# Optimization experiments

Measured on AMD Instinct MI355X. Metric: run time of the kernel, lower is better.

Reference implementation:

```python
import jax, jax.numpy as jnp
import numpy as np

D, H, DH = 64, 4, 32
INNER = H * DH
SCALE = 1.0 / np.sqrt(DH)


def _layernorm(x, w, b, eps=1e-5):
    mu = jnp.mean(x, axis=-1, keepdims=True)
    var = jnp.var(x, axis=-1, keepdims=True)
    return (x - mu) * jax.lax.rsqrt(var + eps) * w + b


def setup_inputs() -> dict:
    key = jax.random.key(0)
    ks = jax.random.split(key, 8)
    B, N = 1, 256
    z = jax.random.normal(ks[0], (B, N, N, D), dtype=jnp.float32)
    mask = jax.random.randint(ks[1], (B, N, N), 0, 2).astype(jnp.bool_)
    ln_w = jnp.ones((D,), jnp.float32)
    ln_b = jnp.zeros((D,), jnp.float32)
    w_qkv = jax.random.normal(ks[2], (3 * INNER, D), jnp.float32) * 0.02
    w_bias = jax.random.normal(ks[3], (H, D), jnp.float32) * 0.02
    w_out = jax.random.normal(ks[4], (D, INNER), jnp.float32) * 0.02
    w_gate = jax.random.normal(ks[5], (INNER, D), jnp.float32) * 0.02
    return {"z": z, "mask": mask, "ln_w": ln_w, "ln_b": ln_b,
            "w_qkv": w_qkv, "w_bias": w_bias, "w_out": w_out, "w_gate": w_gate}


def reference(z, mask, ln_w, ln_b, w_qkv, w_bias, w_out, w_gate):
    # mode == 'starting': attend along the second pair axis per row n.
    B, N = z.shape[0], z.shape[1]
    h = _layernorm(z, ln_w, ln_b)                       # [B,N,N,D]
    qkv = jnp.einsum('bijd,ed->bije', h, w_qkv)         # [B,N,N,3*INNER]
    qkv = qkv.reshape(B, N, N, 3, H, DH)
    q, k, v = qkv[..., 0, :, :], qkv[..., 1, :, :], qkv[..., 2, :, :]  # [B,N,N,H,dh]
    attn = jnp.einsum('bnihd,bnjhd->bnhij', q, k) * SCALE  # [B,N,H,N,N]
    bias = jnp.einsum('bijd,hd->bhij', h, w_bias)          # [B,H,N,N]
    attn = attn + bias[:, None]                            # broadcast over n
    big_neg = jnp.finfo(attn.dtype).min
    attn = jnp.where(mask[:, :, None, None, :], attn, big_neg)  # mask keys j per (b,n)
    attn = jax.nn.softmax(attn, axis=-1)
    out = jnp.einsum('bnhij,bnjhd->bnihd', attn, v)        # [B,N,N,H,dh]
    out = out.reshape(B, N, N, INNER)
    gate = jax.nn.sigmoid(jnp.einsum('bijd,ed->bije', h, w_gate))
    out = jnp.einsum('bije,de->bijd', out * gate, w_out)
    return out
```

## Files before the change

### kernel.cpp

```cpp
#include <hip/hip_runtime.h>
#include <hip/hip_bf16.h>

#define N_ 256
#define D_ 64
#define H_ 4
#define DH_ 32
#define EQKV 384
#define NPOS 65536
#define SCALE_F 0.17677669529663687f
#define BIG_NEG -3.402823466e38f
#define P_STRIDE 264
#define H_STRIDE 72
#define X_STRIDE 136
#define A_STRIDE 136
#define O_STRIDE 68
#define Q_STRIDE 392

typedef __attribute__((ext_vector_type(8))) short s16x8;
typedef __attribute__((ext_vector_type(4))) float f32x4;


__device__ inline short bfbits(float x) {
    __hip_bfloat16 b = __float2bfloat16(x);
    return *reinterpret_cast<short*>(&b);
}
__device__ inline float b2f(short s) {
    unsigned u = ((unsigned)(unsigned short)s) << 16;
    union { unsigned u; float f; } c; c.u = u; return c.f;
}
__device__ inline s16x8 cvt8(float4 a, float4 b) {
    s16x8 r;
    r[0] = bfbits(a.x); r[1] = bfbits(a.y); r[2] = bfbits(a.z); r[3] = bfbits(a.w);
    r[4] = bfbits(b.x); r[5] = bfbits(b.y); r[6] = bfbits(b.z); r[7] = bfbits(b.w);
    return r;
}

__global__ __launch_bounds__(512) void k1_ln_proj_mfma(
    const float* __restrict__ z, const float* __restrict__ ln_w, const float* __restrict__ ln_b,
    const float* __restrict__ w_qkv, const float* __restrict__ w_bias,
    __hip_bfloat16* __restrict__ qkv_ws, __hip_bfloat16* __restrict__ h_ws,
    float* __restrict__ bias_ws)
{
    __shared__ __align__(16) short smem[64 * Q_STRIDE];
    const int t = threadIdx.x;
    const int wave = t >> 6, lane = t & 63;
    const int pos0 = blockIdx.x * 64;
    const int m = lane & 15, quad = lane >> 4;

    {
        const float lw = ln_w[lane], lb = ln_b[lane];
        const float wb0 = w_bias[lane], wb1 = w_bias[64 + lane],
                    wb2 = w_bias[128 + lane], wb3 = w_bias[192 + lane];
        for (int pp = 0; pp < 8; ++pp) {
            const int p = wave * 8 + pp;
            const float zv = z[(size_t)(pos0 + p) * 64 + lane];
            float s = zv, s2 = zv * zv;
            #pragma unroll
            for (int off = 32; off; off >>= 1) { s += __shfl_xor(s, off); s2 += __shfl_xor(s2, off); }
            const float mu = s * 0.015625f;
            const float var = s2 * 0.015625f - mu * mu;
            const float rs = rsqrtf(var + 1e-5f);
            const float hv = (zv - mu) * rs * lw + lb;
            smem[p * H_STRIDE + lane] = bfbits(hv);
            float b0 = hv * wb0, b1 = hv * wb1, b2 = hv * wb2, b3 = hv * wb3;
            #pragma unroll
            for (int off = 32; off; off >>= 1) {
                b0 += __shfl_xor(b0, off); b1 += __shfl_xor(b1, off);
                b2 += __shfl_xor(b2, off); b3 += __shfl_xor(b3, off);
            }
            if (lane < 4) {
                const int gpos = pos0 + p;
                const int gi = gpos >> 8, gj = gpos & 255;
                const float bv = lane == 0 ? b0 : lane == 1 ? b1 : lane == 2 ? b2 : b3;
                bias_ws[lane * NPOS + gj * 256 + gi] = bv;
            }
        }
    }
    __syncthreads();

    {
        const int row = t >> 3, c8 = (t & 7) * 8;
        *(s16x8*)(h_ws + (size_t)(pos0 + row) * 64 + c8) =
            *(const s16x8*)(smem + row * H_STRIDE + c8);
    }

    const int colbase = wave * 48;
    s16x8 bfrag[3][2];
    #pragma unroll
    for (int nt = 0; nt < 3; ++nt) {
        const int col = colbase + nt * 16 + m;
        const float* wp = w_qkv + (size_t)col * 64;
        #pragma unroll
        for (int kt = 0; kt < 2; ++kt) {
            const float4 w0 = *(const float4*)(wp + kt * 32 + quad * 8);
            const float4 w1 = *(const float4*)(wp + kt * 32 + quad * 8 + 4);
            bfrag[nt][kt] = cvt8(w0, w1);
        }
    }

    s16x8 afrag[4][2];
    #pragma unroll
    for (int mt = 0; mt < 4; ++mt)
        #pragma unroll
        for (int kt = 0; kt < 2; ++kt)
            afrag[mt][kt] = *(const s16x8*)(smem + (mt * 16 + m) * H_STRIDE + kt * 32 + quad * 8);

    f32x4 acc[4][3];
    #pragma unroll
    for (int mt = 0; mt < 4; ++mt)
        #pragma unroll
        for (int nt = 0; nt < 3; ++nt)
            acc[mt][nt] = (f32x4){0.f, 0.f, 0.f, 0.f};

    #pragma unroll
    for (int kt = 0; kt < 2; ++kt)
        #pragma unroll
        for (int mt = 0; mt < 4; ++mt)
            #pragma unroll
            for (int nt = 0; nt < 3; ++nt)
                acc[mt][nt] = __builtin_amdgcn_mfma_f32_16x16x32_bf16(
                    afrag[mt][kt], bfrag[nt][kt], acc[mt][nt], 0, 0, 0);

    __syncthreads();

    #pragma unroll
    for (int mt = 0; mt < 4; ++mt)
        #pragma unroll
        for (int nt = 0; nt < 3; ++nt) {
            const int c = colbase + nt * 16 + m;
            #pragma unroll
            for (int r = 0; r < 4; ++r) {
                const int row = mt * 16 + quad * 4 + r;
                smem[row * Q_STRIDE + c] = bfbits(acc[mt][nt][r]);
            }
        }
    __syncthreads();

    #pragma unroll
    for (int i = 0; i < 6; ++i) {
        const int idx = i * 512 + t;
        const int row = idx / 48, c8 = (idx % 48) * 8;
        *(s16x8*)(qkv_ws + (size_t)(pos0 + row) * EQKV + c8) =
            *(const s16x8*)(smem + row * Q_STRIDE + c8);
    }
}

__global__ __launch_bounds__(512, 4) void k2_attn_mfma(
    const __hip_bfloat16* __restrict__ qkv_ws, const float* __restrict__ bias_ws,
    const int* __restrict__ mask, __hip_bfloat16* __restrict__ attn_bf)
{
    __shared__ __align__(16) short p_s[64 * P_STRIDE];
    __shared__ __align__(16) short vt_s[32 * P_STRIDE];
    __shared__ float keep[256];
    __shared__ float redl[64][2];

    const int bx = blockIdx.x;
    const int n = bx & 255, h = bx >> 8;
    const int t = threadIdx.x;
    const int wave = t >> 6, lane = t & 63;
    const int m = lane & 15, quad = lane >> 4;
    const int mt = wave & 3, nh = wave >> 2;

    if (t < 256) keep[t] = (mask[n * 256 + t] != 0) ? 1.0f : 0.0f;

    {
        const int j = t >> 1, dh = (t & 1) * 16;
        const __hip_bfloat16* vp = qkv_ws + (size_t)(n * 256 + j) * 384 + 256 + h * 32 + dh;
        s16x8 v0 = *(const s16x8*)vp;
        s16x8 v1 = *(const s16x8*)(vp + 8);
        #pragma unroll
        for (int e = 0; e < 8; ++e) {
            vt_s[(dh + e) * P_STRIDE + j]     = v0[e];
            vt_s[(dh + 8 + e) * P_STRIDE + j] = v1[e];
        }
    }

    s16x8 kf[8];
    #pragma unroll
    for (int tt = 0; tt < 8; ++tt) {
        const int jt = nh * 8 + tt;
        kf[tt] = *(const s16x8*)(qkv_ws + (size_t)(n * 256 + jt * 16 + m) * 384 + 128 + h * 32 + quad * 8);
    }
    __syncthreads();

    for (int ig = 0; ig < 4; ++ig) {
        const int i0 = ig * 64;
        const int ibase = i0 + mt * 16 + quad * 4;

        f32x4 s[8];
        {
            const size_t qbase = (size_t)(n * 256 + i0 + mt * 16 + m) * 384 + h * 32 + quad * 8;
            const s16x8 afrag = *(const s16x8*)(qkv_ws + qbase);
            #pragma unroll
            for (int tt = 0; tt < 8; ++tt) {
                f32x4 z4 = {0.f, 0.f, 0.f, 0.f};
                s[tt] = __builtin_amdgcn_mfma_f32_16x16x32_bf16(afrag, kf[tt], z4, 0, 0, 0);
            }
        }
        #pragma unroll
        for (int tt = 0; tt < 8; ++tt) {
            const int j = (nh * 8 + tt) * 16 + m;
            const float kp = keep[j];
            const float4 b4 = *(const float4*)(bias_ws + (size_t)h * NPOS + j * 256 + ibase);
            const float* bp = reinterpret_cast<const float*>(&b4);
            #pragma unroll
            for (int r = 0; r < 4; ++r) {
                const float sv = s[tt][r] * SCALE_F + bp[r];
                s[tt][r] = (kp != 0.f) ? sv : BIG_NEG;
            }
        }

        {
            float ls[4];
            #pragma unroll
            for (int r = 0; r < 4; ++r) {
                float acc = 0.f;
                #pragma unroll
                for (int tt = 0; tt < 8; ++tt) {
                    const float p = __expf(s[tt][r]);
                    s[tt][r] = p;
                    acc += p;
                }
                #pragma unroll
                for (int off = 1; off < 16; off <<= 1) acc += __shfl_xor(acc, off);
                ls[r] = acc;
            }
            if (m == 0) {
                #pragma unroll
                for (int r = 0; r < 4; ++r) redl[mt * 16 + quad * 4 + r][nh] = ls[r];
            }
            #pragma unroll
            for (int tt = 0; tt < 8; ++tt) {
                const int col = (nh * 8 + tt) * 16 + m;
                #pragma unroll
                for (int r = 0; r < 4; ++r) {
                    const int row = mt * 16 + quad * 4 + r;
                    p_s[row * P_STRIDE + col] = bfbits(s[tt][r]);
                }
            }
        }
        __syncthreads();

        {
            f32x4 o = {0.f, 0.f, 0.f, 0.f};
            const int arow = mt * 16 + m;
            const int brow = nh * 16 + m;
            #pragma unroll
            for (int kt = 0; kt < 8; ++kt) {
                const s16x8 ap = *(const s16x8*)(p_s + arow * P_STRIDE + kt * 32 + quad * 8);
                const s16x8 bv = *(const s16x8*)(vt_s + brow * P_STRIDE + kt * 32 + quad * 8);
                o = __builtin_amdgcn_mfma_f32_16x16x32_bf16(ap, bv, o, 0, 0, 0);
            }
            #pragma unroll
            for (int r = 0; r < 4; ++r) {
                const int row = mt * 16 + quad * 4 + r;
                const float l = fmaxf(redl[row][0] + redl[row][1], 1e-30f);
                const float val = o[r] * (1.0f / l);
                const int ig_row = i0 + row;
                attn_bf[(size_t)(n * 256 + ig_row) * 128 + h * 32 + nh * 16 + m] = __float2bfloat16(val);
            }
        }
        __syncthreads();
    }
}

__global__ __launch_bounds__(512) void k3_proj_mfma(
    const __hip_bfloat16* __restrict__ attn_bf, const __hip_bfloat16* __restrict__ h_ws,
    const float* __restrict__ w_gate, const float* __restrict__ w_out, float* __restrict__ out)
{
    __shared__ __align__(16) short h_s[64 * H_STRIDE];
    __shared__ __align__(16) short a_s[64 * A_STRIDE];
    __shared__ __align__(16) short x_s[64 * X_STRIDE];
    const int t = threadIdx.x;
    const int wave = t >> 6, lane = t & 63;
    const int pos0 = blockIdx.x * 64;
    const int m = lane & 15, quad = lane >> 4;

    {
        const int row = t >> 3, c8 = (t & 7) * 8;
        *(s16x8*)(h_s + row * H_STRIDE + c8) =
            *(const s16x8*)(h_ws + (size_t)(pos0 + row) * 64 + c8);
    }
    #pragma unroll
    for (int i = 0; i < 2; ++i) {
        const int idx = i * 512 + t;
        const int row = idx >> 4, c8 = (idx & 15) * 8;
        *(s16x8*)(a_s + row * A_STRIDE + c8) =
            *(const s16x8*)(attn_bf + (size_t)(pos0 + row) * 128 + c8);
    }
    __syncthreads();

    {
        const int mt = wave & 3, cg = wave >> 2;
        s16x8 ha[2];
        #pragma unroll
        for (int kt = 0; kt < 2; ++kt)
            ha[kt] = *(const s16x8*)(h_s + (mt * 16 + m) * H_STRIDE + kt * 32 + quad * 8);
        #pragma unroll
        for (int nt = 0; nt < 4; ++nt) {
            const float* wp = w_gate + (size_t)(cg * 64 + nt * 16 + m) * 64;
            const s16x8 b0 = cvt8(*(const float4*)(wp + quad * 8),
                                  *(const float4*)(wp + quad * 8 + 4));
            const s16x8 b1 = cvt8(*(const float4*)(wp + 32 + quad * 8),
                                  *(const float4*)(wp + 32 + quad * 8 + 4));
            f32x4 g4 = (f32x4){0.f, 0.f, 0.f, 0.f};
            g4 = __builtin_amdgcn_mfma_f32_16x16x32_bf16(ha[0], b0, g4, 0, 0, 0);
            g4 = __builtin_amdgcn_mfma_f32_16x16x32_bf16(ha[1], b1, g4, 0, 0, 0);
            const int col = cg * 64 + nt * 16 + m;
            #pragma unroll
            for (int r = 0; r < 4; ++r) {
                const int row = mt * 16 + quad * 4 + r;
                const float gv = 1.0f / (1.0f + __expf(-g4[r]));
                x_s[row * X_STRIDE + col] = bfbits(b2f(a_s[row * A_STRIDE + col]) * gv);
            }
        }
    }
    __syncthreads();

    const int mt = wave & 3, nh = wave >> 2;
    s16x8 bfrag[2][4];
    #pragma unroll
    for (int nt = 0; nt < 2; ++nt) {
        const int d = nh * 32 + nt * 16 + m;
        const float* wp = w_out + (size_t)d * 128;
        #pragma unroll
        for (int kt = 0; kt < 4; ++kt) {
            const float4 w0 = *(const float4*)(wp + kt * 32 + quad * 8);
            const float4 w1 = *(const float4*)(wp + kt * 32 + quad * 8 + 4);
            bfrag[nt][kt] = cvt8(w0, w1);
        }
    }

    s16x8 afrag[4];
    #pragma unroll
    for (int kt = 0; kt < 4; ++kt)
        afrag[kt] = *(const s16x8*)(x_s + (mt * 16 + m) * X_STRIDE + kt * 32 + quad * 8);

    f32x4 acc[2];
    acc[0] = (f32x4){0.f, 0.f, 0.f, 0.f};
    acc[1] = (f32x4){0.f, 0.f, 0.f, 0.f};
    #pragma unroll
    for (int kt = 0; kt < 4; ++kt) {
        acc[0] = __builtin_amdgcn_mfma_f32_16x16x32_bf16(afrag[kt], bfrag[0][kt], acc[0], 0, 0, 0);
        acc[1] = __builtin_amdgcn_mfma_f32_16x16x32_bf16(afrag[kt], bfrag[1][kt], acc[1], 0, 0, 0);
    }

    float* o_s = (float*)a_s;
    #pragma unroll
    for (int nt = 0; nt < 2; ++nt) {
        const int d = nh * 32 + nt * 16 + m;
        #pragma unroll
        for (int r = 0; r < 4; ++r) {
            const int row = mt * 16 + quad * 4 + r;
            o_s[row * O_STRIDE + d] = acc[nt][r];
        }
    }
    __syncthreads();

    #pragma unroll
    for (int i = 0; i < 2; ++i) {
        const int idx = i * 512 + t;
        const int row = idx >> 4, c4 = (idx & 15) * 4;
        *(float4*)(out + (size_t)(pos0 + row) * 64 + c4) =
            *(const float4*)(o_s + row * O_STRIDE + c4);
    }
}

extern "C" void kernel_launch(void* const* d_in, const int* in_sizes, int n_in,
                              void* d_out, int out_size, void* d_ws, size_t ws_size,
                              hipStream_t stream) {
    const float* z      = (const float*)d_in[0];
    const int*   mask   = (const int*)d_in[1];
    const float* ln_w   = (const float*)d_in[2];
    const float* ln_b   = (const float*)d_in[3];
    const float* w_qkv  = (const float*)d_in[4];
    const float* w_bias = (const float*)d_in[5];
    const float* w_out  = (const float*)d_in[6];
    const float* w_gate = (const float*)d_in[7];
    float* out = (float*)d_out;

    char* ws = (char*)d_ws;
    __hip_bfloat16* qkv_ws  = (__hip_bfloat16*)(ws);
    float*          bias_ws = (float*)(ws + 50331648);
    __hip_bfloat16* h_ws    = (__hip_bfloat16*)(ws + 51380224);
    __hip_bfloat16* attn_bf = (__hip_bfloat16*)(ws + 59768832);

    k1_ln_proj_mfma<<<1024, 512, 0, stream>>>(z, ln_w, ln_b, w_qkv, w_bias,
                                              qkv_ws, h_ws, bias_ws);
    k2_attn_mfma<<<1024, 512, 0, stream>>>(qkv_ws, bias_ws, mask, attn_bf);
    k3_proj_mfma<<<1024, 512, 0, stream>>>(attn_bf, h_ws, w_gate, w_out, out);
}
```

Measured before the change: 209.4 us.

## Transpose bias layout, prefetch next Q and bias, split PV accumulators

```diff
diff --git a/kernel.cpp b/kernel.cpp
--- a/kernel.cpp
+++ b/kernel.cpp
@@ -72,7 +72,7 @@
                 const int gpos = pos0 + p;
                 const int gi = gpos >> 8, gj = gpos & 255;
                 const float bv = lane == 0 ? b0 : lane == 1 ? b1 : lane == 2 ? b2 : b3;
-                bias_ws[lane * NPOS + gj * 256 + gi] = bv;
+                bias_ws[lane * NPOS + gi * 256 + gj] = bv;
             }
         }
     }
@@ -181,31 +181,34 @@
         const int jt = nh * 8 + tt;
         kf[tt] = *(const s16x8*)(qkv_ws + (size_t)(n * 256 + jt * 16 + m) * 384 + 128 + h * 32 + quad * 8);
     }
+
+    const int jcol0 = nh * 128 + m;
+    const float* bias_h = bias_ws + (size_t)h * NPOS;
+    s16x8 qf = *(const s16x8*)(qkv_ws + (size_t)(n * 256 + mt * 16 + m) * 384 + h * 32 + quad * 8);
+    float bb[8][4];
+    #pragma unroll
+    for (int tt = 0; tt < 8; ++tt)
+        #pragma unroll
+        for (int r = 0; r < 4; ++r)
+            bb[tt][r] = bias_h[(mt * 16 + quad * 4 + r) * 256 + jcol0 + tt * 16];
+
     __syncthreads();
 
     for (int ig = 0; ig < 4; ++ig) {
         const int i0 = ig * 64;
-        const int ibase = i0 + mt * 16 + quad * 4;
 
         f32x4 s[8];
-        {
-            const size_t qbase = (size_t)(n * 256 + i0 + mt * 16 + m) * 384 + h * 32 + quad * 8;
-            const s16x8 afrag = *(const s16x8*)(qkv_ws + qbase);
-            #pragma unroll
-            for (int tt = 0; tt < 8; ++tt) {
-                f32x4 z4 = {0.f, 0.f, 0.f, 0.f};
-                s[tt] = __builtin_amdgcn_mfma_f32_16x16x32_bf16(afrag, kf[tt], z4, 0, 0, 0);
-            }
-        }
         #pragma unroll
         for (int tt = 0; tt < 8; ++tt) {
-            const int j = (nh * 8 + tt) * 16 + m;
-            const float kp = keep[j];
-            const float4 b4 = *(const float4*)(bias_ws + (size_t)h * NPOS + j * 256 + ibase);
-            const float* bp = reinterpret_cast<const float*>(&b4);
+            f32x4 z4 = {0.f, 0.f, 0.f, 0.f};
+            s[tt] = __builtin_amdgcn_mfma_f32_16x16x32_bf16(qf, kf[tt], z4, 0, 0, 0);
+        }
+        #pragma unroll
+        for (int tt = 0; tt < 8; ++tt) {
+            const float kp = keep[jcol0 + tt * 16];
             #pragma unroll
             for (int r = 0; r < 4; ++r) {
-                const float sv = s[tt][r] * SCALE_F + bp[r];
+                const float sv = s[tt][r] * SCALE_F + bb[tt][r];
                 s[tt][r] = (kp != 0.f) ? sv : BIG_NEG;
             }
         }
@@ -239,23 +242,37 @@
                 }
             }
         }
+
+        if (ig < 3) {
+            const int i0n = i0 + 64;
+            qf = *(const s16x8*)(qkv_ws + (size_t)(n * 256 + i0n + mt * 16 + m) * 384 + h * 32 + quad * 8);
+            #pragma unroll
+            for (int tt = 0; tt < 8; ++tt)
+                #pragma unroll
+                for (int r = 0; r < 4; ++r)
+                    bb[tt][r] = bias_h[(i0n + mt * 16 + quad * 4 + r) * 256 + jcol0 + tt * 16];
+        }
         __syncthreads();
 
         {
-            f32x4 o = {0.f, 0.f, 0.f, 0.f};
+            f32x4 o0 = {0.f, 0.f, 0.f, 0.f};
+            f32x4 o1 = {0.f, 0.f, 0.f, 0.f};
             const int arow = mt * 16 + m;
             const int brow = nh * 16 + m;
             #pragma unroll
-            for (int kt = 0; kt < 8; ++kt) {
-                const s16x8 ap = *(const s16x8*)(p_s + arow * P_STRIDE + kt * 32 + quad * 8);
-                const s16x8 bv = *(const s16x8*)(vt_s + brow * P_STRIDE + kt * 32 + quad * 8);
-                o = __builtin_amdgcn_mfma_f32_16x16x32_bf16(ap, bv, o, 0, 0, 0);
+            for (int kt = 0; kt < 4; ++kt) {
+                const s16x8 ap0 = *(const s16x8*)(p_s + arow * P_STRIDE + (2 * kt) * 32 + quad * 8);
+                const s16x8 bv0 = *(const s16x8*)(vt_s + brow * P_STRIDE + (2 * kt) * 32 + quad * 8);
+                o0 = __builtin_amdgcn_mfma_f32_16x16x32_bf16(ap0, bv0, o0, 0, 0, 0);
+                const s16x8 ap1 = *(const s16x8*)(p_s + arow * P_STRIDE + (2 * kt + 1) * 32 + quad * 8);
+                const s16x8 bv1 = *(const s16x8*)(vt_s + brow * P_STRIDE + (2 * kt + 1) * 32 + quad * 8);
+                o1 = __builtin_amdgcn_mfma_f32_16x16x32_bf16(ap1, bv1, o1, 0, 0, 0);
             }
             #pragma unroll
             for (int r = 0; r < 4; ++r) {
                 const int row = mt * 16 + quad * 4 + r;
                 const float l = fmaxf(redl[row][0] + redl[row][1], 1e-30f);
-                const float val = o[r] * (1.0f / l);
+                const float val = (o0[r] + o1[r]) * (1.0f / l);
                 const int ig_row = i0 + row;
                 attn_bf[(size_t)(n * 256 + ig_row) * 128 + h * 32 + nh * 16 + m] = __float2bfloat16(val);
             }
```

New measurement: 197.4 us. -5.7%, faster.

## Give each wave private query rows to drop block-wide barriers in attention

Applied to the files above, without the earlier changes.

```diff
diff --git a/kernel.cpp b/kernel.cpp
--- a/kernel.cpp
+++ b/kernel.cpp
@@ -10,6 +10,7 @@
 #define SCALE_F 0.17677669529663687f
 #define BIG_NEG -3.402823466e38f
 #define P_STRIDE 264
+#define PPS 136
 #define H_STRIDE 72
 #define X_STRIDE 136
 #define A_STRIDE 136
@@ -145,21 +146,19 @@
     }
 }
 
-__global__ __launch_bounds__(512, 4) void k2_attn_mfma(
+__global__ __launch_bounds__(512, 6) void k2_attn_mfma(
     const __hip_bfloat16* __restrict__ qkv_ws, const float* __restrict__ bias_ws,
     const int* __restrict__ mask, __hip_bfloat16* __restrict__ attn_bf)
 {
-    __shared__ __align__(16) short p_s[64 * P_STRIDE];
     __shared__ __align__(16) short vt_s[32 * P_STRIDE];
     __shared__ float keep[256];
-    __shared__ float redl[64][2];
-
+    __shared__ __align__(16) short p_pv[8][16 * PPS];
     const int bx = blockIdx.x;
     const int n = bx & 255, h = bx >> 8;
     const int t = threadIdx.x;
     const int wave = t >> 6, lane = t & 63;
     const int m = lane & 15, quad = lane >> 4;
-    const int mt = wave & 3, nh = wave >> 2;
+    short* pp = &p_pv[wave][0];
 
     if (t < 256) keep[t] = (mask[n * 256 + t] != 0) ? 1.0f : 0.0f;
 
@@ -174,93 +173,59 @@
             vt_s[(dh + 8 + e) * P_STRIDE + j] = v1[e];
         }
     }
-
-    s16x8 kf[8];
-    #pragma unroll
-    for (int tt = 0; tt < 8; ++tt) {
-        const int jt = nh * 8 + tt;
-        kf[tt] = *(const s16x8*)(qkv_ws + (size_t)(n * 256 + jt * 16 + m) * 384 + 128 + h * 32 + quad * 8);
-    }
-    __syncthreads();
-
-    for (int ig = 0; ig < 4; ++ig) {
-        const int i0 = ig * 64;
-        const int ibase = i0 + mt * 16 + quad * 4;
-
-        f32x4 s[8];
-        {
-            const size_t qbase = (size_t)(n * 256 + i0 + mt * 16 + m) * 384 + h * 32 + quad * 8;
-            const s16x8 afrag = *(const s16x8*)(qkv_ws + qbase);
+    __syncthreads();
+
+    const __hip_bfloat16* qrow = qkv_ws + (size_t)n * 256 * 384;
+    const float* bias_hT = bias_ws + (size_t)h * NPOS;
+
+    for (int set = 0; set < 2; ++set) {
+        const int i0 = set * 128 + wave * 16;
+        const s16x8 qf = *(const s16x8*)(qrow + (size_t)(i0 + m) * 384 + h * 32 + quad * 8);
+        f32x4 o0 = {0.f, 0.f, 0.f, 0.f};
+        f32x4 o1 = {0.f, 0.f, 0.f, 0.f};
+        float lsum = 0.f;
+
+        #pragma unroll
+        for (int jh = 0; jh < 2; ++jh) {
+            const int jb = jh * 128;
             #pragma unroll
             for (int tt = 0; tt < 8; ++tt) {
+                const int jt = jb + tt * 16;
+                const s16x8 kf = *(const s16x8*)(qrow + (size_t)(jt + m) * 384 + 128 + h * 32 + quad * 8);
                 f32x4 z4 = {0.f, 0.f, 0.f, 0.f};
-                s[tt] = __builtin_amdgcn_mfma_f32_16x16x32_bf16(afrag, kf[tt], z4, 0, 0, 0);
-            }
-        }
-        #pragma unroll
-        for (int tt = 0; tt < 8; ++tt) {
-            const int j = (nh * 8 + tt) * 16 + m;
-            const float kp = keep[j];
-            const float4 b4 = *(const float4*)(bias_ws + (size_t)h * NPOS + j * 256 + ibase);
-            const float* bp = reinterpret_cast<const float*>(&b4);
-            #pragma unroll
-            for (int r = 0; r < 4; ++r) {
-                const float sv = s[tt][r] * SCALE_F + bp[r];
-                s[tt][r] = (kp != 0.f) ? sv : BIG_NEG;
-            }
-        }
-
-        {
-            float ls[4];
-            #pragma unroll
-            for (int r = 0; r < 4; ++r) {
-                float acc = 0.f;
-                #pragma unroll
-                for (int tt = 0; tt < 8; ++tt) {
-                    const float p = __expf(s[tt][r]);
-                    s[tt][r] = p;
-                    acc += p;
-                }
-                #pragma unroll
-                for (int off = 1; off < 16; off <<= 1) acc += __shfl_xor(acc, off);
-                ls[r] = acc;
-            }
-            if (m == 0) {
-                #pragma unroll
-                for (int r = 0; r < 4; ++r) redl[mt * 16 + quad * 4 + r][nh] = ls[r];
-            }
-            #pragma unroll
-            for (int tt = 0; tt < 8; ++tt) {
-                const int col = (nh * 8 + tt) * 16 + m;
+                const f32x4 sv = __builtin_amdgcn_mfma_f32_16x16x32_bf16(kf, qf, z4, 0, 0, 0);
                 #pragma unroll
                 for (int r = 0; r < 4; ++r) {
-                    const int row = mt * 16 + quad * 4 + r;
-                    p_s[row * P_STRIDE + col] = bfbits(s[tt][r]);
+                    const int j = jt + quad * 4 + r;
+                    const float bvv = bias_hT[(size_t)j * 256 + i0 + m];
+                    const float x = (keep[j] != 0.f) ? (sv[r] * SCALE_F + bvv) : BIG_NEG;
+                    const float p = __expf(x);
+                    lsum += p;
+                    pp[m * PPS + tt * 16 + quad * 4 + r] = bfbits(p);
                 }
             }
-        }
-        __syncthreads();
-
-        {
-            f32x4 o = {0.f, 0.f, 0.f, 0.f};
-            const int arow = mt * 16 + m;
-            const int brow = nh * 16 + m;
-            #pragma unroll
-            for (int kt = 0; kt < 8; ++kt) {
-                const s16x8 ap = *(const s16x8*)(p_s + arow * P_STRIDE + kt * 32 + quad * 8);
-                const s16x8 bv = *(const s16x8*)(vt_s + brow * P_STRIDE + kt * 32 + quad * 8);
-                o = __builtin_amdgcn_mfma_f32_16x16x32_bf16(ap, bv, o, 0, 0, 0);
-            }
-            #pragma unroll
-            for (int r = 0; r < 4; ++r) {
-                const int row = mt * 16 + quad * 4 + r;
-                const float l = fmaxf(redl[row][0] + redl[row][1], 1e-30f);
-                const float val = o[r] * (1.0f / l);
-                const int ig_row = i0 + row;
-                attn_bf[(size_t)(n * 256 + ig_row) * 128 + h * 32 + nh * 16 + m] = __float2bfloat16(val);
-            }
-        }
-        __syncthreads();
+            #pragma unroll
+            for (int kt = 0; kt < 4; ++kt) {
+                const s16x8 ap  = *(const s16x8*)(pp + m * PPS + kt * 32 + quad * 8);
+                const s16x8 bv0 = *(const s16x8*)(vt_s + m * P_STRIDE + jb + kt * 32 + quad * 8);
+                o0 = __builtin_amdgcn_mfma_f32_16x16x32_bf16(ap, bv0, o0, 0, 0, 0);
+                const s16x8 bv1 = *(const s16x8*)(vt_s + (16 + m) * P_STRIDE + jb + kt * 32 + quad * 8);
+                o1 = __builtin_amdgcn_mfma_f32_16x16x32_bf16(ap, bv1, o1, 0, 0, 0);
+            }
+        }
+
+        lsum += __shfl_xor(lsum, 16);
+        lsum += __shfl_xor(lsum, 32);
+
+        #pragma unroll
+        for (int r = 0; r < 4; ++r) {
+            const float lr = __shfl(lsum, quad * 4 + r);
+            const float linv = 1.0f / fmaxf(lr, 1e-30f);
+            const int row = i0 + quad * 4 + r;
+            __hip_bfloat16* op = attn_bf + (size_t)(n * 256 + row) * 128 + h * 32;
+            op[m]      = __float2bfloat16(o0[r] * linv);
+            op[16 + m] = __float2bfloat16(o1[r] * linv);
+        }
     }
 }
 
```

New measurement: 545.2 us. +160.3%, slower.
